# Kernel optimization log

Hardware: AMD Instinct MI355X
Metric: run time of the kernel (lower is better)

The kernel has to match this reference:

```python
import jax, jax.numpy as jnp
import numpy as np
from jax import lax

E = 3  # num_experts

def _maxpool2(x):
    return lax.reduce_window(x, -jnp.inf, lax.max, (1, 1, 2, 2), (1, 1, 2, 2), 'VALID')

def _mixed_conv(x, experts, routing, stride, pad):
    # per-sample expert-mixed convolution via grouped conv trick
    B, Ci, H, W = x.shape
    _, Co, _, k, _ = experts.shape
    kern = jnp.einsum('be,eoikl->boikl', routing, experts).reshape(B * Co, Ci, k, k)
    y = lax.conv_general_dilated(
        x.reshape(1, B * Ci, H, W), kern, (stride, stride),
        [(pad, pad), (pad, pad)],
        dimension_numbers=('NCHW', 'OIHW', 'NCHW'),
        feature_group_count=B)
    return y.reshape(B, Co, y.shape[2], y.shape[3])

def _dyres_conv(x, experts, rw, rb, stride=1, pad=1):
    # DyRes mode 'A': routing from avg-pool + spatial-std descriptors, softmax over experts
    avg = x.mean((2, 3))
    std = x.std((2, 3))
    r = jax.nn.softmax((avg + std) @ rw.T + rb, axis=-1)  # [B, E]
    return _mixed_conv(x, experts, r, stride, pad)

def _cond_conv(x, experts, rw, rb, stride=1, pad=1):
    # CondConv: sigmoid routing from global average pool
    r = jax.nn.sigmoid(x.mean((2, 3)) @ rw.T + rb)  # [B, E]
    return _mixed_conv(x, experts, r, stride, pad)

def _conv_init(key, co, ci, k):
    return jax.random.normal(key, (E, co, ci, k, k), jnp.float32) * np.sqrt(2.0 / (ci * k * k)).astype(np.float32)

def setup_inputs() -> dict:
    key = jax.random.key(0)
    ks = jax.random.split(key, 20)
    B = 512
    d = {}
    d['x'] = jax.random.normal(ks[0], (B, 3, 32, 32), jnp.float32)
    d['dw1'] = _conv_init(ks[1], 64, 3, 3)
    d['rw1'] = jax.random.normal(ks[2], (E, 3), jnp.float32) * 0.1
    d['rb1'] = jnp.zeros((E,), jnp.float32)
    d['dw2'] = _conv_init(ks[3], 192, 64, 3)
    d['rw2'] = jax.random.normal(ks[4], (E, 64), jnp.float32) * 0.1
    d['rb2'] = jnp.zeros((E,), jnp.float32)
    d['dw3'] = _conv_init(ks[5], 384, 192, 3)
    d['rw3'] = jax.random.normal(ks[6], (E, 192), jnp.float32) * 0.1
    d['rb3'] = jnp.zeros((E,), jnp.float32)
    d['cw4'] = _conv_init(ks[7], 256, 384, 3)
    d['cr4w'] = jax.random.normal(ks[8], (E, 384), jnp.float32) * 0.1
    d['cr4b'] = jnp.zeros((E,), jnp.float32)
    d['cw5'] = _conv_init(ks[9], 256, 256, 3)
    d['cr5w'] = jax.random.normal(ks[10], (E, 256), jnp.float32) * 0.1
    d['cr5b'] = jnp.zeros((E,), jnp.float32)
    d['fw1'] = jax.random.normal(ks[11], (4096, 1024), jnp.float32) * np.sqrt(2.0 / 1024).astype(np.float32)
    d['fb1'] = jnp.zeros((4096,), jnp.float32)
    d['fw2'] = jax.random.normal(ks[12], (4096, 4096), jnp.float32) * np.sqrt(2.0 / 4096).astype(np.float32)
    d['fb2'] = jnp.zeros((4096,), jnp.float32)
    d['fw3'] = jax.random.normal(ks[13], (100, 4096), jnp.float32) * np.sqrt(1.0 / 4096).astype(np.float32)
    d['fb3'] = jnp.zeros((100,), jnp.float32)
    return d

def reference(x, dw1, rw1, rb1, dw2, rw2, rb2, dw3, rw3, rb3,
              cw4, cr4w, cr4b, cw5, cr5w, cr5b,
              fw1, fb1, fw2, fb2, fw3, fb3):
    h = jax.nn.relu(_dyres_conv(x, dw1, rw1, rb1, stride=2))   # [B,64,16,16]
    h = _maxpool2(h)                                           # [B,64,8,8]
    h = jax.nn.relu(_dyres_conv(h, dw2, rw2, rb2))             # [B,192,8,8]
    h = _maxpool2(h)                                           # [B,192,4,4]
    h = jax.nn.relu(_dyres_conv(h, dw3, rw3, rb3))             # [B,384,4,4]
    h = jax.nn.relu(_cond_conv(h, cw4, cr4w, cr4b))            # [B,256,4,4]
    h = jax.nn.relu(_cond_conv(h, cw5, cr5w, cr5b))            # [B,256,4,4]
    h = _maxpool2(h)                                           # [B,256,2,2]
    h = h.reshape(h.shape[0], -1)                              # [B,1024]
    h = jax.nn.relu(h @ fw1.T + fb1)
    h = jax.nn.relu(h @ fw2.T + fb2)
    return h @ fw3.T + fb3                                     # [B,100]
```

## Files before the change

kernel.cpp:

```cpp
#include <hip/hip_runtime.h>
#include <math.h>


typedef unsigned short u16;
typedef unsigned int u32;
typedef short bf16x8 __attribute__((ext_vector_type(8)));
typedef short bf16x4 __attribute__((ext_vector_type(4)));
typedef float f32x4 __attribute__((ext_vector_type(4)));

__device__ __forceinline__ u16 bf16_rne(float f) {
    u32 u = __float_as_uint(f);
    return (u16)((u + 0x7fffu + ((u >> 16) & 1u)) >> 16);
}
__device__ __forceinline__ u32 packsplit(float v) {
    u16 h = bf16_rne(v);
    float hf = __uint_as_float((u32)h << 16);
    u16 l = bf16_rne(v - hf);
    return ((u32)h << 16) | l;
}
__device__ __forceinline__ float unpackf(u32 p) {
    return __uint_as_float(p & 0xffff0000u) + __uint_as_float(p << 16);
}
__device__ __forceinline__ int xcd_swz(int bid, int n) {
    if ((n & 7) != 0) return bid;
    int cpx = n >> 3;
    return (bid & 7) * cpx + (bid >> 3);
}

#if __has_builtin(__builtin_amdgcn_mfma_f32_16x16x16bf16_1k)
__device__ __forceinline__ f32x4 mfma16(bf16x4 a, bf16x4 b, f32x4 c) {
    return __builtin_amdgcn_mfma_f32_16x16x16bf16_1k(a, b, c, 0, 0, 0);
}
#else
__device__ __forceinline__ f32x4 mfma16(bf16x4 a, bf16x4 b, f32x4 c) {
    bf16x8 az = {a[0], a[1], a[2], a[3], (short)0, (short)0, (short)0, (short)0};
    bf16x8 bz = {b[0], b[1], b[2], b[3], (short)0, (short)0, (short)0, (short)0};
    return __builtin_amdgcn_mfma_f32_16x16x32_bf16(az, bz, c, 0, 0, 0);
}
#endif

__global__ __launch_bounds__(256)
void wsplit_kernel(const float* __restrict__ W, u16* __restrict__ whi,
                   u16* __restrict__ wlo, int total, int Kper, int Kpad)
{
    int idx = blockIdx.x * 256 + threadIdx.x;
    if (idx >= total) return;
    int r = idx / Kpad, k = idx - r * Kpad;
    float v = (k < Kper) ? W[(size_t)r * Kper + k] : 0.f;
    u16 h = bf16_rne(v);
    whi[idx] = h;
    wlo[idx] = bf16_rne(v - __uint_as_float((u32)h << 16));
}

__global__ __launch_bounds__(256)
void wsplit_cl_kernel(const float* __restrict__ W, u16* __restrict__ whi,
                      u16* __restrict__ wlo, int total, int Ci)
{
    int idx = blockIdx.x * 256 + threadIdx.x;
    if (idx >= total) return;
    int Kper = 9 * Ci;
    int r = idx / Kper, kp = idx - r * Kper;
    int cell = kp / Ci, ci = kp - cell * Ci;
    float v = W[(size_t)r * Kper + ci * 9 + cell];
    u16 h = bf16_rne(v);
    whi[idx] = h;
    wlo[idx] = bf16_rne(v - __uint_as_float((u32)h << 16));
}

__global__ __launch_bounds__(64)
void stats_kernel(const float* __restrict__ actv, float* __restrict__ s,
                  int C, int HW, int use_std)
{
    int idx = blockIdx.x;
    size_t base = (size_t)idx * HW;
    int lane = threadIdx.x;
    float sum = 0.f, sq = 0.f;
    const float* p = actv + base;
    for (int i = lane; i < HW; i += 64) { float v = p[i]; sum += v; sq += v * v; }
#pragma unroll
    for (int off = 32; off > 0; off >>= 1) {
        sum += __shfl_down(sum, off);
        sq  += __shfl_down(sq, off);
    }
    if (lane == 0) {
        float inv = 1.f / (float)HW;
        float mean = sum * inv;
        float var = sq * inv - mean * mean;
        float outv = mean;
        if (use_std) outv += sqrtf(fmaxf(var, 0.f));
        s[idx] = outv;
    }
}

__global__ __launch_bounds__(384)
void stats_cl_kernel(const u32* __restrict__ act, float* __restrict__ s,
                     int H2, int W2, int C, int use_std)
{
    int b = blockIdx.x, c = threadIdx.x;
    int Hin = H2 - 2, Win = W2 - 2;
    float sum = 0.f, sq = 0.f;
    for (int h = 0; h < Hin; ++h)
        for (int w = 0; w < Win; ++w) {
            float v = unpackf(act[(((size_t)b * H2 + h + 1) * W2 + w + 1) * C + c]);
            sum += v; sq += v * v;
        }
    float inv = 1.f / (float)(Hin * Win);
    float mean = sum * inv;
    float var = sq * inv - mean * mean;
    float outv = mean;
    if (use_std) outv += sqrtf(fmaxf(var, 0.f));
    s[b * C + c] = outv;
}

__global__ __launch_bounds__(64)
void routing_kernel(const float* __restrict__ s, const float* __restrict__ rw,
                    const float* __restrict__ rb, float* __restrict__ r,
                    int C, int softmax_mode)
{
    int b = blockIdx.x;
    int lane = threadIdx.x;
    float d0 = 0.f, d1 = 0.f, d2 = 0.f;
    for (int c = lane; c < C; c += 64) {
        float sv = s[b * C + c];
        d0 += sv * rw[c];
        d1 += sv * rw[C + c];
        d2 += sv * rw[2 * C + c];
    }
#pragma unroll
    for (int off = 32; off > 0; off >>= 1) {
        d0 += __shfl_down(d0, off);
        d1 += __shfl_down(d1, off);
        d2 += __shfl_down(d2, off);
    }
    if (lane == 0) {
        d0 += rb[0]; d1 += rb[1]; d2 += rb[2];
        if (softmax_mode) {
            float mx = fmaxf(d0, fmaxf(d1, d2));
            float e0 = expf(d0 - mx), e1 = expf(d1 - mx), e2 = expf(d2 - mx);
            float inv = 1.f / (e0 + e1 + e2);
            r[b * 3 + 0] = e0 * inv;
            r[b * 3 + 1] = e1 * inv;
            r[b * 3 + 2] = e2 * inv;
        } else {
            r[b * 3 + 0] = 1.f / (1.f + expf(-d0));
            r[b * 3 + 1] = 1.f / (1.f + expf(-d1));
            r[b * 3 + 2] = 1.f / (1.f + expf(-d2));
        }
    }
}

template<int CI, int H2, int W2, int LGS, int LGOW>
__global__ __launch_bounds__(256, 3)
void cgemm_cl_kernel(const u16* __restrict__ Whi, const u16* __restrict__ Wlo,
                     const u32* __restrict__ Bpk, const float* __restrict__ rptr,
                     float* __restrict__ Cout, int M, int N, int Kper, int Kchunk)
{
    __shared__ __align__(16) u16 Ah[2][128 * 20], Al[2][128 * 20];
    __shared__ __align__(16) u16 Bh[2][128 * 20], Bl[2][128 * 20];
    const int tid = threadIdx.x;
    const int bx = xcd_swz(blockIdx.x, gridDim.x);
    const int n0 = bx << 7, m0 = blockIdx.y << 7;
    const int kq0 = blockIdx.z * Kchunk;

    const int rowA = tid >> 1, kh8 = (tid & 1) << 3;
    const int nBr = tid >> 1, kOffB = (tid & 1) << 3;

    const int nn = n0 + nBr;
    const int bB = nn >> LGS;
    const int sidx = nn & ((1 << LGS) - 1);
    const int oh = sidx >> LGOW, ow = sidx & ((1 << LGOW) - 1);
    const long nBase = ((long)(bB * H2 + oh) * W2 + ow) * CI;
    const float rsB0 = rptr[bB * 3 + 0];
    const float rsB1 = rptr[bB * 3 + 1];
    const float rsB2 = rptr[bB * 3 + 2];

    const int lane = tid & 63, wv = tid >> 6;
    const int lm = lane & 15, qd = lane >> 4;
    const int wm = (wv & 1) << 6, wn = (wv >> 1) << 6;

    f32x4 acc[4][4];
#pragma unroll
    for (int i = 0; i < 4; ++i)
#pragma unroll
        for (int j = 0; j < 4; ++j)
            acc[i][j] = (f32x4){0.f, 0.f, 0.f, 0.f};

    const int mg = m0 + rowA;
    const int nkz = Kchunk >> 4;
    const int NS = 3 * nkz;

    int eL = 0, kL = kq0;
    uint4 pAh, pAl;
    uint4 pQ0, pQ1;

    auto LOAD = [&]() {
        size_t aOff = ((size_t)(eL * M + mg)) * Kper + kL + kh8;
        pAh = *(const uint4*)(Whi + aOff);
        pAl = *(const uint4*)(Wlo + aOff);
        int k = kL + kOffB;
        int cell = k / CI;
        int ci0 = k - cell * CI;
        int kh = (cell * 11) >> 5;
        int kw = cell - kh * 3;
        const u32* bp = Bpk + (nBase + (long)((kh * W2 + kw) * CI + ci0));
        pQ0 = *(const uint4*)bp;
        pQ1 = *(const uint4*)(bp + 4);
    };
    auto ADV = [&]() {
        kL += 16;
        if (kL == kq0 + Kchunk) { kL = kq0; ++eL; }
    };
    auto STORE = [&](int buf, float rs) {
        *(uint4*)(&Ah[buf][rowA * 20 + kh8]) = pAh;
        *(uint4*)(&Al[buf][rowA * 20 + kh8]) = pAl;
        u32 qv[8] = {pQ0.x, pQ0.y, pQ0.z, pQ0.w, pQ1.x, pQ1.y, pQ1.z, pQ1.w};
        u32 sv[8];
#pragma unroll
        for (int j = 0; j < 8; ++j)
            sv[j] = packsplit(unpackf(qv[j]) * rs);
        u32 hw[4], lw[4];
#pragma unroll
        for (int j = 0; j < 4; ++j) {
            u32 p0 = sv[2 * j], p1 = sv[2 * j + 1];
            hw[j] = (p0 >> 16) | (p1 & 0xffff0000u);
            lw[j] = (p0 & 0xffffu) | (p1 << 16);
        }
        *(uint4*)(&Bh[buf][nBr * 20 + kOffB]) = make_uint4(hw[0], hw[1], hw[2], hw[3]);
        *(uint4*)(&Bl[buf][nBr * 20 + kOffB]) = make_uint4(lw[0], lw[1], lw[2], lw[3]);
    };
    auto COMPUTE = [&](int buf) {
        bf16x4 ah[4], al[4];
#pragma unroll
        for (int mi = 0; mi < 4; ++mi) {
            int off = (wm + mi * 16 + lm) * 20 + qd * 4;
            ah[mi] = *(const bf16x4*)(&Ah[buf][off]);
            al[mi] = *(const bf16x4*)(&Al[buf][off]);
        }
        __builtin_amdgcn_s_setprio(1);
#pragma unroll
        for (int ni = 0; ni < 4; ++ni) {
            int off = (wn + ni * 16 + lm) * 20 + qd * 4;
            bf16x4 bh = *(const bf16x4*)(&Bh[buf][off]);
            bf16x4 bl = *(const bf16x4*)(&Bl[buf][off]);
#pragma unroll
            for (int mi = 0; mi < 4; ++mi) {
                f32x4 c = acc[mi][ni];
                c = mfma16(al[mi], bh, c);
                c = mfma16(ah[mi], bl, c);
                c = mfma16(ah[mi], bh, c);
                acc[mi][ni] = c;
            }
        }
        __builtin_amdgcn_s_setprio(0);
    };

    LOAD(); ADV();
    int s = 0, buf = 0;
#pragma unroll
    for (int e = 0; e < 3; ++e) {
        const float rs = (e == 0) ? rsB0 : ((e == 1) ? rsB1 : rsB2);
        for (int t = 0; t < nkz; ++t) {
            STORE(buf, rs);
            if (s + 1 < NS) { LOAD(); ADV(); }
            asm volatile("s_waitcnt lgkmcnt(0)\n\ts_barrier" ::: "memory");
            COMPUTE(buf);
            buf ^= 1; ++s;
        }
    }

    const bool atom = (gridDim.z > 1);
#pragma unroll
    for (int ni = 0; ni < 4; ++ni) {
        int n = n0 + wn + ni * 16 + lm;
#pragma unroll
        for (int mi = 0; mi < 4; ++mi)
#pragma unroll
            for (int r = 0; r < 4; ++r) {
                int m = m0 + wm + mi * 16 + qd * 4 + r;
                if (m >= M) continue;
                float v = acc[mi][ni][r];
                if (atom) atomicAdd(&Cout[(size_t)n * M + m], v);
                else      Cout[(size_t)n * M + m] = v;
            }
    }
}

__global__ __launch_bounds__(256, 2)
void cgemm_l1_kernel(const u16* __restrict__ Whi, const u16* __restrict__ Wlo,
                     const u32* __restrict__ Bpk, const float* __restrict__ rptr,
                     float* __restrict__ Cout, int M, int N)
{
    __shared__ __align__(16) u16 Ah[2][128 * 40], Al[2][128 * 40];
    __shared__ __align__(16) u16 Bh[2][128 * 40], Bl[2][128 * 40];
    const int tid = threadIdx.x;
    const int bx = xcd_swz(blockIdx.x, gridDim.x);
    const int n0 = bx << 7;
    const int Kper = 27, Kpad = 32;
    const int H = 32, W = 32;

    const int rowA = tid >> 1, kh16 = (tid & 1) << 4;
    const int nB = tid & 127, kOff = (tid >> 7) << 4;

    const int nn = n0 + nB;
    const int bB = nn >> 8;
    const int sidx = nn & 255;
    const int ohs = (sidx >> 4) * 2 - 1;
    const int ows = (sidx & 15) * 2 - 1;
    const long nBase = (long)bB * 3072 + (long)ohs * W + ows;

    const int lane = tid & 63, wv = tid >> 6;
    const int lm = lane & 15, qd = lane >> 4;
    const int wm = (wv & 1) << 6, wn = (wv >> 1) << 6;

    float rsv[3][4];
#pragma unroll
    for (int ni = 0; ni < 4; ++ni) {
        int n = n0 + wn + ni * 16 + lm;
        int b = n >> 8;
#pragma unroll
        for (int e = 0; e < 3; ++e) rsv[e][ni] = rptr[b * 3 + e];
    }

    f32x4 acc[4][4], accS[4][4];
#pragma unroll
    for (int i = 0; i < 4; ++i)
#pragma unroll
        for (int j = 0; j < 4; ++j) {
            acc[i][j]  = (f32x4){0.f, 0.f, 0.f, 0.f};
            accS[i][j] = (f32x4){0.f, 0.f, 0.f, 0.f};
        }

    const int mg = rowA;
    int eL = 0;
    uint4 pA0, pA1, pA2, pA3;
    u32 pB[16];

    auto LOAD = [&]() {
        size_t aOff = ((size_t)(eL * M + mg)) * Kpad + kh16;
        const u16* hp = Whi + aOff;
        const u16* lp = Wlo + aOff;
        pA0 = *(const uint4*)hp; pA1 = *(const uint4*)(hp + 8);
        pA2 = *(const uint4*)lp; pA3 = *(const uint4*)(lp + 8);
#pragma unroll
        for (int j = 0; j < 16; ++j) {
            int k = kOff + j;
            int ci = (int)((unsigned)k / 9u);
            int r9 = k - ci * 9;
            int kh = (int)(((unsigned)r9 * 11u) >> 5);
            int kw = r9 - kh * 3;
            int ih = ohs + kh, iw = ows + kw;
            u32 p = 0;
            if (k < Kper && (unsigned)ih < (unsigned)H && (unsigned)iw < (unsigned)W)
                p = Bpk[nBase + (long)ci * 1024 + kh * W + kw];
            pB[j] = p;
        }
    };
    auto STORE = [&](int buf) {
        *(uint4*)(&Ah[buf][rowA * 40 + kh16])     = pA0;
        *(uint4*)(&Ah[buf][rowA * 40 + kh16 + 8]) = pA1;
        *(uint4*)(&Al[buf][rowA * 40 + kh16])     = pA2;
        *(uint4*)(&Al[buf][rowA * 40 + kh16 + 8]) = pA3;
        u32 hw[8], lw[8];
#pragma unroll
        for (int j = 0; j < 8; ++j) {
            u32 p0 = pB[2 * j], p1 = pB[2 * j + 1];
            hw[j] = (p0 >> 16) | (p1 & 0xffff0000u);
            lw[j] = (p0 & 0xffffu) | (p1 << 16);
        }
        *(uint4*)(&Bh[buf][nB * 40 + kOff])     = make_uint4(hw[0], hw[1], hw[2], hw[3]);
        *(uint4*)(&Bh[buf][nB * 40 + kOff + 8]) = make_uint4(hw[4], hw[5], hw[6], hw[7]);
        *(uint4*)(&Bl[buf][nB * 40 + kOff])     = make_uint4(lw[0], lw[1], lw[2], lw[3]);
        *(uint4*)(&Bl[buf][nB * 40 + kOff + 8]) = make_uint4(lw[4], lw[5], lw[6], lw[7]);
    };
    auto COMPUTE = [&](int buf) {
        bf16x8 ah[4], al[4];
#pragma unroll
        for (int mi = 0; mi < 4; ++mi) {
            int row = wm + mi * 16 + lm;
            ah[mi] = *(const bf16x8*)(&Ah[buf][row * 40 + qd * 8]);
            al[mi] = *(const bf16x8*)(&Al[buf][row * 40 + qd * 8]);
        }
        __builtin_amdgcn_s_setprio(1);
#pragma unroll
        for (int ni = 0; ni < 4; ++ni) {
            int row = wn + ni * 16 + lm;
            bf16x8 bh = *(const bf16x8*)(&Bh[buf][row * 40 + qd * 8]);
            bf16x8 bl = *(const bf16x8*)(&Bl[buf][row * 40 + qd * 8]);
#pragma unroll
            for (int mi = 0; mi < 4; ++mi) {
                f32x4 c = acc[mi][ni];
                c = __builtin_amdgcn_mfma_f32_16x16x32_bf16(al[mi], bh, c, 0, 0, 0);
                c = __builtin_amdgcn_mfma_f32_16x16x32_bf16(ah[mi], bl, c, 0, 0, 0);
                c = __builtin_amdgcn_mfma_f32_16x16x32_bf16(ah[mi], bh, c, 0, 0, 0);
                acc[mi][ni] = c;
            }
        }
        __builtin_amdgcn_s_setprio(0);
    };

    LOAD(); ++eL;
    int buf = 0;
#pragma unroll
    for (int e = 0; e < 3; ++e) {
        STORE(buf);
        if (e < 2) { LOAD(); ++eL; }
        asm volatile("s_waitcnt lgkmcnt(0)\n\ts_barrier" ::: "memory");
        COMPUTE(buf);
        buf ^= 1;
#pragma unroll
        for (int mi = 0; mi < 4; ++mi)
#pragma unroll
            for (int ni = 0; ni < 4; ++ni) {
                accS[mi][ni] += acc[mi][ni] * rsv[e][ni];
                acc[mi][ni] = (f32x4){0.f, 0.f, 0.f, 0.f};
            }
    }

#pragma unroll
    for (int ni = 0; ni < 4; ++ni) {
        int n = n0 + wn + ni * 16 + lm;
#pragma unroll
        for (int mi = 0; mi < 4; ++mi)
#pragma unroll
            for (int r = 0; r < 4; ++r) {
                int m = wm + mi * 16 + qd * 4 + r;
                if (m >= M) continue;
                Cout[(size_t)n * M + m] = accS[mi][ni][r];
            }
    }
}

template<int BIAS, int TROUT>
__global__ __launch_bounds__(256, 2)
void mgemm_kernel(const u16* __restrict__ Whi, const u16* __restrict__ Wlo,
                  const u32* __restrict__ Bpk, const float* __restrict__ bias,
                  float* __restrict__ Cout,
                  int M, int N, int Kpad, int Kchunk)
{
    __shared__ __align__(16) u16 Ah[2][128 * 40], Al[2][128 * 40];
    __shared__ __align__(16) u32 Bp[2][128 * 36];
    const int tid = threadIdx.x;
    const int n0 = blockIdx.x << 7, m0 = blockIdx.y << 7;
    const int bz = blockIdx.z;
    const int kq0 = bz * Kchunk;
    const int kEnd = kq0 + Kchunk;

    const int rowA = tid >> 1, kh16 = (tid & 1) << 4;
    const int nB = tid & 127, kOff = (tid >> 7) << 4;

    const int lane = tid & 63, wv = tid >> 6;
    const int lm = lane & 15, qd = lane >> 4;
    const int wm = (wv & 1) << 6, wn = (wv >> 1) << 6;

    f32x4 acc[4][4];
#pragma unroll
    for (int i = 0; i < 4; ++i)
#pragma unroll
        for (int j = 0; j < 4; ++j)
            acc[i][j] = (f32x4){0.f, 0.f, 0.f, 0.f};

    const int mg = m0 + rowA;
    uint4 pA0, pA1, pA2, pA3;
    uint4 pQ0, pQ1, pQ2, pQ3;

    auto LOAD = [&](int kq) {
        if (mg < M) {
            const u16* hp = Whi + (size_t)mg * Kpad + kq + kh16;
            const u16* lp = Wlo + (size_t)mg * Kpad + kq + kh16;
            pA0 = *(const uint4*)hp; pA1 = *(const uint4*)(hp + 8);
            pA2 = *(const uint4*)lp; pA3 = *(const uint4*)(lp + 8);
        } else {
            pA0 = make_uint4(0,0,0,0); pA1 = make_uint4(0,0,0,0);
            pA2 = make_uint4(0,0,0,0); pA3 = make_uint4(0,0,0,0);
        }
        const u32* bp = Bpk + (size_t)(n0 + nB) * Kpad + kq + kOff;
        pQ0 = *(const uint4*)bp;
        pQ1 = *(const uint4*)(bp + 4);
        pQ2 = *(const uint4*)(bp + 8);
        pQ3 = *(const uint4*)(bp + 12);
    };
    auto STORE = [&](int buf) {
        *(uint4*)(&Ah[buf][rowA * 40 + kh16])     = pA0;
        *(uint4*)(&Ah[buf][rowA * 40 + kh16 + 8]) = pA1;
        *(uint4*)(&Al[buf][rowA * 40 + kh16])     = pA2;
        *(uint4*)(&Al[buf][rowA * 40 + kh16 + 8]) = pA3;
        u32* bp = &Bp[buf][nB * 36 + kOff];
        *(uint4*)(bp)      = pQ0;
        *(uint4*)(bp + 4)  = pQ1;
        *(uint4*)(bp + 8)  = pQ2;
        *(uint4*)(bp + 12) = pQ3;
    };
    auto COMPUTE = [&](int buf) {
        bf16x8 ah[4], al[4];
#pragma unroll
        for (int mi = 0; mi < 4; ++mi) {
            int row = wm + mi * 16 + lm;
            ah[mi] = *(const bf16x8*)(&Ah[buf][row * 40 + qd * 8]);
            al[mi] = *(const bf16x8*)(&Al[buf][row * 40 + qd * 8]);
        }
        __builtin_amdgcn_s_setprio(1);
#pragma unroll
        for (int ni = 0; ni < 4; ++ni) {
            const u32* bp = &Bp[buf][(wn + ni * 16 + lm) * 36 + qd * 8];
            uint4 p0 = *(const uint4*)bp;
            uint4 p1 = *(const uint4*)(bp + 4);
            union { u32 w[4]; bf16x8 v; } bh, bl;
            bh.w[0] = (p0.x >> 16) | (p0.y & 0xffff0000u);
            bl.w[0] = (p0.x & 0xffffu) | (p0.y << 16);
            bh.w[1] = (p0.z >> 16) | (p0.w & 0xffff0000u);
            bl.w[1] = (p0.z & 0xffffu) | (p0.w << 16);
            bh.w[2] = (p1.x >> 16) | (p1.y & 0xffff0000u);
            bl.w[2] = (p1.x & 0xffffu) | (p1.y << 16);
            bh.w[3] = (p1.z >> 16) | (p1.w & 0xffff0000u);
            bl.w[3] = (p1.z & 0xffffu) | (p1.w << 16);
#pragma unroll
            for (int mi = 0; mi < 4; ++mi) {
                f32x4 c = acc[mi][ni];
                c = __builtin_amdgcn_mfma_f32_16x16x32_bf16(al[mi], bh.v, c, 0, 0, 0);
                c = __builtin_amdgcn_mfma_f32_16x16x32_bf16(ah[mi], bl.v, c, 0, 0, 0);
                c = __builtin_amdgcn_mfma_f32_16x16x32_bf16(ah[mi], bh.v, c, 0, 0, 0);
                acc[mi][ni] = c;
            }
        }
        __builtin_amdgcn_s_setprio(0);
    };

    LOAD(kq0);
    int buf = 0;
    for (int kq = kq0; kq < kEnd; kq += 32) {
        STORE(buf);
        if (kq + 32 < kEnd) LOAD(kq + 32);
        asm volatile("s_waitcnt lgkmcnt(0)\n\ts_barrier" ::: "memory");
        COMPUTE(buf);
        buf ^= 1;
    }

#pragma unroll
    for (int ni = 0; ni < 4; ++ni) {
        int n = n0 + wn + ni * 16 + lm;
        if (n >= N) continue;
#pragma unroll
        for (int mi = 0; mi < 4; ++mi)
#pragma unroll
            for (int r = 0; r < 4; ++r) {
                int m = m0 + wm + mi * 16 + qd * 4 + r;
                if (m >= M) continue;
                float v = acc[mi][ni][r];
                if (BIAS && bz == 0) v += bias[m];
                if (TROUT) atomicAdd(&Cout[(size_t)n * M + m], v);
                else       atomicAdd(&Cout[(size_t)m * N + n], v);
            }
    }
}

__global__ __launch_bounds__(256)
void pack_kernel(const float* __restrict__ in, u32* __restrict__ outp, int count)
{
    int i = blockIdx.x * 256 + threadIdx.x;
    if (i >= count) return;
    outp[i] = packsplit(in[i]);
}

__global__ __launch_bounds__(256)
void pool_pack_cl_kernel(const float* __restrict__ in, u32* __restrict__ outp,
                         int Bn, int Hin, int Win, int C)
{
    int OH = Hin >> 1, OW = Win >> 1, H2 = OH + 2, W2 = OW + 2;
    int total = Bn * H2 * W2 * C;
    int i = blockIdx.x * 256 + threadIdx.x;
    if (i >= total) return;
    int c = i % C; int t = i / C;
    int w = t % W2; t /= W2;
    int h = t % H2; int b = t / H2;
    u32 pv = 0;
    if (h >= 1 && h <= OH && w >= 1 && w <= OW) {
        int oh = h - 1, ow = w - 1;
        const float* p = in + (((size_t)b * Hin + 2 * oh) * Win + 2 * ow) * C + c;
        size_t rs = (size_t)Win * C;
        float v = fmaxf(fmaxf(p[0], p[C]), fmaxf(p[rs], p[rs + C]));
        pv = packsplit(fmaxf(v, 0.f));
    }
    outp[i] = pv;
}

__global__ __launch_bounds__(256)
void pack_cl_kernel(const float* __restrict__ in, u32* __restrict__ outp,
                    int Bn, int Hin, int Win, int C)
{
    int H2 = Hin + 2, W2 = Win + 2;
    int total = Bn * H2 * W2 * C;
    int i = blockIdx.x * 256 + threadIdx.x;
    if (i >= total) return;
    int c = i % C; int t = i / C;
    int w = t % W2; t /= W2;
    int h = t % H2; int b = t / H2;
    u32 pv = 0;
    if (h >= 1 && h <= Hin && w >= 1 && w <= Win) {
        float v = in[(((size_t)b * Hin + (h - 1)) * Win + (w - 1)) * C + c];
        pv = packsplit(fmaxf(v, 0.f));
    }
    outp[i] = pv;
}

__global__ __launch_bounds__(256)
void pool_flatten_cl_kernel(const float* __restrict__ in, u32* __restrict__ outp)
{
    int i = blockIdx.x * 256 + threadIdx.x;
    if (i >= 512 * 1024) return;
    int b = i >> 10;
    int f = i & 1023;
    int c = f >> 2, sp = f & 3;
    int oh = sp >> 1, ow = sp & 1;
    const float* p = in + (((size_t)b * 4 + 2 * oh) * 4 + 2 * ow) * 256 + c;
    float v = fmaxf(fmaxf(p[0], p[256]), fmaxf(p[1024], p[1024 + 256]));
    outp[i] = packsplit(fmaxf(v, 0.f));
}

__global__ __launch_bounds__(256)
void tp_pack_kernel(const float* __restrict__ in, u32* __restrict__ outp,
                    int Mt, int Nt)
{
    __shared__ float t[32][33];
    int tx = threadIdx.x & 31, ty = threadIdx.x >> 5;
    int mB = blockIdx.x << 5, nB = blockIdx.y << 5;
#pragma unroll
    for (int i = 0; i < 4; ++i) {
        int mm = ty + i * 8;
        t[mm][tx] = in[(size_t)(mB + mm) * Nt + nB + tx];
    }
    __syncthreads();
#pragma unroll
    for (int i = 0; i < 4; ++i) {
        int nn = ty + i * 8;
        float v = fmaxf(t[tx][nn], 0.f);
        outp[(size_t)(nB + nn) * Mt + mB + tx] = packsplit(v);
    }
}

extern "C" void kernel_launch(void* const* d_in, const int* in_sizes, int n_in,
                              void* d_out, int out_size, void* d_ws, size_t ws_size,
                              hipStream_t stream)
{
    const float* x    = (const float*)d_in[0];
    const float* dw1  = (const float*)d_in[1];
    const float* rw1  = (const float*)d_in[2];
    const float* rb1  = (const float*)d_in[3];
    const float* dw2  = (const float*)d_in[4];
    const float* rw2  = (const float*)d_in[5];
    const float* rb2  = (const float*)d_in[6];
    const float* dw3  = (const float*)d_in[7];
    const float* rw3  = (const float*)d_in[8];
    const float* rb3  = (const float*)d_in[9];
    const float* cw4  = (const float*)d_in[10];
    const float* cr4w = (const float*)d_in[11];
    const float* cr4b = (const float*)d_in[12];
    const float* cw5  = (const float*)d_in[13];
    const float* cr5w = (const float*)d_in[14];
    const float* cr5b = (const float*)d_in[15];
    const float* fw1  = (const float*)d_in[16];
    const float* fb1  = (const float*)d_in[17];
    const float* fw2  = (const float*)d_in[18];
    const float* fb2  = (const float*)d_in[19];
    const float* fw3  = (const float*)d_in[20];
    const float* fb3  = (const float*)d_in[21];
    float* out = (float*)d_out;

    float* ws    = (float*)d_ws;
    float* r1    = ws;
    float* r2    = r1 + 1536;
    float* r3    = r2 + 1536;
    float* r4    = r3 + 1536;
    float* r5    = r4 + 1536;
    float* sdesc = ws + 8192 + 65536;
    const size_t REGION = 18874368;
    float* region = sdesc + 196608;
    float* slab   = region;
    u32*   a3u    = (u32*)(region + 4194304);
    u16*   regEnd = (u16*)(region + REGION);
    u32*   P1     = (u32*)(region + REGION);

    u16 *w1h = regEnd - 2*(size_t)6144,     *w1l = regEnd - (size_t)6144;
    u16 *w2h = regEnd - 2*(size_t)331776,   *w2l = regEnd - (size_t)331776;
    u16 *w3h = regEnd - 2*(size_t)1990656,  *w3l = regEnd - (size_t)1990656;
    u16 *w4h = regEnd - 2*(size_t)2654208,  *w4l = regEnd - (size_t)2654208;
    u16 *w5h = regEnd - 2*(size_t)1769472,  *w5l = regEnd - (size_t)1769472;
    u16 *f1h = regEnd - 2*(size_t)4194304,  *f1l = regEnd - (size_t)4194304;
    u16 *f2h = regEnd - 2*(size_t)16777216, *f2l = regEnd - (size_t)16777216;
    u16 *f3h = regEnd - 2*(size_t)409600,   *f3l = regEnd - (size_t)409600;

    u32* xpk   = P1;
    u32* a1    = P1;
    u32* a2    = P1;
    u32* a4    = P1;
    u32* hTpk  = P1;
    u32* f1pkT = P1 + 1048576;
    u32* f2pkT = P1 + 3145728;

    const int B = 512;

    pack_kernel<<<6144, 256, 0, stream>>>(x, xpk, 1572864);

    wsplit_kernel<<<24, 256, 0, stream>>>(dw1, w1h, w1l, 6144, 27, 32);
    stats_kernel<<<B * 3, 64, 0, stream>>>(x, sdesc, 3, 1024, 1);
    routing_kernel<<<B, 64, 0, stream>>>(sdesc, rw1, rb1, r1, 3, 1);
    cgemm_l1_kernel<<<dim3(1024, 1, 1), 256, 0, stream>>>(
        w1h, w1l, xpk, r1, slab, 64, 131072);
    pool_pack_cl_kernel<<<12800, 256, 0, stream>>>(slab, a1, B, 16, 16, 64);

    wsplit_cl_kernel<<<1296, 256, 0, stream>>>(dw2, w2h, w2l, 331776, 64);
    stats_cl_kernel<<<B, 64, 0, stream>>>(a1, sdesc, 10, 10, 64, 1);
    routing_kernel<<<B, 64, 0, stream>>>(sdesc, rw2, rb2, r2, 64, 1);
    hipMemsetAsync(slab, 0, (size_t)192 * 32768 * 4, stream);
    cgemm_cl_kernel<64, 10, 10, 6, 3><<<dim3(256, 2, 2), 256, 0, stream>>>(
        w2h, w2l, a1, r2, slab, 192, 32768, 576, 288);
    pool_pack_cl_kernel<<<13824, 256, 0, stream>>>(slab, a2, B, 8, 8, 192);

    wsplit_cl_kernel<<<7776, 256, 0, stream>>>(dw3, w3h, w3l, 1990656, 192);
    stats_cl_kernel<<<B, 192, 0, stream>>>(a2, sdesc, 6, 6, 192, 1);
    routing_kernel<<<B, 64, 0, stream>>>(sdesc, rw3, rb3, r3, 192, 1);
    hipMemsetAsync(slab, 0, (size_t)8192 * 384 * 4, stream);
    cgemm_cl_kernel<192, 6, 6, 4, 2><<<dim3(64, 3, 4), 256, 0, stream>>>(
        w3h, w3l, a2, r3, slab, 384, 8192, 1728, 432);
    pack_cl_kernel<<<27648, 256, 0, stream>>>(slab, a3u, B, 4, 4, 384);

    wsplit_cl_kernel<<<10368, 256, 0, stream>>>(cw4, w4h, w4l, 2654208, 384);
    stats_cl_kernel<<<B, 384, 0, stream>>>(a3u, sdesc, 6, 6, 384, 0);
    routing_kernel<<<B, 64, 0, stream>>>(sdesc, cr4w, cr4b, r4, 384, 0);
    hipMemsetAsync(slab, 0, (size_t)8192 * 256 * 4, stream);
    cgemm_cl_kernel<384, 6, 6, 4, 2><<<dim3(64, 2, 6), 256, 0, stream>>>(
        w4h, w4l, a3u, r4, slab, 256, 8192, 3456, 576);
    pack_cl_kernel<<<18432, 256, 0, stream>>>(slab, a4, B, 4, 4, 256);

    wsplit_cl_kernel<<<6912, 256, 0, stream>>>(cw5, w5h, w5l, 1769472, 256);
    stats_cl_kernel<<<B, 256, 0, stream>>>(a4, sdesc, 6, 6, 256, 0);
    routing_kernel<<<B, 64, 0, stream>>>(sdesc, cr5w, cr5b, r5, 256, 0);
    hipMemsetAsync(slab, 0, (size_t)8192 * 256 * 4, stream);
    cgemm_cl_kernel<256, 6, 6, 4, 2><<<dim3(64, 2, 6), 256, 0, stream>>>(
        w5h, w5l, a4, r5, slab, 256, 8192, 2304, 384);

    pool_flatten_cl_kernel<<<2048, 256, 0, stream>>>(slab, hTpk);

    wsplit_kernel<<<16384, 256, 0, stream>>>(fw1, f1h, f1l, 4194304, 1024, 1024);
    hipMemsetAsync(slab, 0, (size_t)4096 * 512 * 4, stream);
    mgemm_kernel<1, 0><<<dim3(4, 32, 8), 256, 0, stream>>>(
        f1h, f1l, hTpk, fb1, slab, 4096, 512, 1024, 128);
    tp_pack_kernel<<<dim3(128, 16), 256, 0, stream>>>(slab, f1pkT, 4096, 512);

    wsplit_kernel<<<65536, 256, 0, stream>>>(fw2, f2h, f2l, 16777216, 4096, 4096);
    hipMemsetAsync(slab, 0, (size_t)4096 * 512 * 4, stream);
    mgemm_kernel<1, 0><<<dim3(4, 32, 8), 256, 0, stream>>>(
        f2h, f2l, f1pkT, fb2, slab, 4096, 512, 4096, 512);
    tp_pack_kernel<<<dim3(128, 16), 256, 0, stream>>>(slab, f2pkT, 4096, 512);

    wsplit_kernel<<<1600, 256, 0, stream>>>(fw3, f3h, f3l, 409600, 4096, 4096);
    hipMemsetAsync(out, 0, (size_t)512 * 100 * 4, stream);
    mgemm_kernel<1, 1><<<dim3(4, 1, 32), 256, 0, stream>>>(
        f3h, f3l, f2pkT, fb3, out, 100, 512, 4096, 128);
}
```

Before: 1.807 ms.

## Use K=32 bf16 MFMA with packed hi/lo weights in conv GEMMs

The conv-layer GEMMs now store weights as packed hi/lo u32 words, produced by a new split kernel. Shared-memory tiles hold packed u32 values that are split into bf16x8 operands at fragment load, so each step can use 16x16x32 MFMAs instead of 16x16x16. The M tile shrinks to 64, the K step doubles to 32, and split-K counts and grids are retuned. Layer 2 drops split-K, along with its memset and atomics. The change cuts MFMA instruction count and global load count, but adds unpacking ALU work in the inner loop and lowers per-block reuse of B.

```diff
diff --git a/kernel.cpp b/kernel.cpp
--- a/kernel.cpp
+++ b/kernel.cpp
@@ -5,7 +5,6 @@
 typedef unsigned short u16;
 typedef unsigned int u32;
 typedef short bf16x8 __attribute__((ext_vector_type(8)));
-typedef short bf16x4 __attribute__((ext_vector_type(4)));
 typedef float f32x4 __attribute__((ext_vector_type(4)));
 
 __device__ __forceinline__ u16 bf16_rne(float f) {
@@ -26,18 +25,6 @@
     int cpx = n >> 3;
     return (bid & 7) * cpx + (bid >> 3);
 }
-
-#if __has_builtin(__builtin_amdgcn_mfma_f32_16x16x16bf16_1k)
-__device__ __forceinline__ f32x4 mfma16(bf16x4 a, bf16x4 b, f32x4 c) {
-    return __builtin_amdgcn_mfma_f32_16x16x16bf16_1k(a, b, c, 0, 0, 0);
-}
-#else
-__device__ __forceinline__ f32x4 mfma16(bf16x4 a, bf16x4 b, f32x4 c) {
-    bf16x8 az = {a[0], a[1], a[2], a[3], (short)0, (short)0, (short)0, (short)0};
-    bf16x8 bz = {b[0], b[1], b[2], b[3], (short)0, (short)0, (short)0, (short)0};
-    return __builtin_amdgcn_mfma_f32_16x16x32_bf16(az, bz, c, 0, 0, 0);
-}
-#endif
 
 __global__ __launch_bounds__(256)
 void wsplit_kernel(const float* __restrict__ W, u16* __restrict__ whi,
@@ -53,18 +40,19 @@
 }
 
 __global__ __launch_bounds__(256)
-void wsplit_cl_kernel(const float* __restrict__ W, u16* __restrict__ whi,
-                      u16* __restrict__ wlo, int total, int Ci)
+void wsplit_clp_kernel(const float* __restrict__ W, u32* __restrict__ wp,
+                       int total, int Ci, int Kpad)
 {
     int idx = blockIdx.x * 256 + threadIdx.x;
     if (idx >= total) return;
     int Kper = 9 * Ci;
-    int r = idx / Kper, kp = idx - r * Kper;
-    int cell = kp / Ci, ci = kp - cell * Ci;
-    float v = W[(size_t)r * Kper + ci * 9 + cell];
-    u16 h = bf16_rne(v);
-    whi[idx] = h;
-    wlo[idx] = bf16_rne(v - __uint_as_float((u32)h << 16));
+    int r = idx / Kpad, k = idx - r * Kpad;
+    u32 p = 0;
+    if (k < Kper) {
+        int cell = k / Ci, ci = k - cell * Ci;
+        p = packsplit(W[(size_t)r * Kper + ci * 9 + cell]);
+    }
+    wp[idx] = p;
 }
 
 __global__ __launch_bounds__(64)
@@ -151,19 +139,19 @@
 
 template<int CI, int H2, int W2, int LGS, int LGOW>
 __global__ __launch_bounds__(256, 3)
-void cgemm_cl_kernel(const u16* __restrict__ Whi, const u16* __restrict__ Wlo,
-                     const u32* __restrict__ Bpk, const float* __restrict__ rptr,
-                     float* __restrict__ Cout, int M, int N, int Kper, int Kchunk)
-{
-    __shared__ __align__(16) u16 Ah[2][128 * 20], Al[2][128 * 20];
-    __shared__ __align__(16) u16 Bh[2][128 * 20], Bl[2][128 * 20];
+void cgemm_cl_kernel(const u32* __restrict__ Apk, const u32* __restrict__ Bpk,
+                     const float* __restrict__ rptr, float* __restrict__ Cout,
+                     int M, int N, int Kper, int Kchunk)
+{
+    __shared__ __align__(16) u32 ApS[2][64 * 34];
+    __shared__ __align__(16) u32 BpS[2][128 * 34];
     const int tid = threadIdx.x;
     const int bx = xcd_swz(blockIdx.x, gridDim.x);
-    const int n0 = bx << 7, m0 = blockIdx.y << 7;
+    const int n0 = bx << 7, m0 = blockIdx.y << 6;
     const int kq0 = blockIdx.z * Kchunk;
 
-    const int rowA = tid >> 1, kh8 = (tid & 1) << 3;
-    const int nBr = tid >> 1, kOffB = (tid & 1) << 3;
+    const int rowA = tid >> 2, kA = (tid & 3) << 3;
+    const int nBr = tid >> 1, kB = (tid & 1) << 4;
 
     const int nn = n0 + nBr;
     const int bB = nn >> LGS;
@@ -176,28 +164,27 @@
 
     const int lane = tid & 63, wv = tid >> 6;
     const int lm = lane & 15, qd = lane >> 4;
-    const int wm = (wv & 1) << 6, wn = (wv >> 1) << 6;
-
-    f32x4 acc[4][4];
-#pragma unroll
-    for (int i = 0; i < 4; ++i)
+    const int wm = (wv & 1) << 5, wn = (wv >> 1) << 6;
+
+    f32x4 acc[2][4];
+#pragma unroll
+    for (int i = 0; i < 2; ++i)
 #pragma unroll
         for (int j = 0; j < 4; ++j)
             acc[i][j] = (f32x4){0.f, 0.f, 0.f, 0.f};
 
-    const int mg = m0 + rowA;
-    const int nkz = Kchunk >> 4;
+    const int nkz = Kchunk >> 5;
     const int NS = 3 * nkz;
 
     int eL = 0, kL = kq0;
-    uint4 pAh, pAl;
-    uint4 pQ0, pQ1;
+    uint4 pA0, pA1;
+    uint4 pQ0, pQ1, pQ2, pQ3;
 
     auto LOAD = [&]() {
-        size_t aOff = ((size_t)(eL * M + mg)) * Kper + kL + kh8;
-        pAh = *(const uint4*)(Whi + aOff);
-        pAl = *(const uint4*)(Wlo + aOff);
-        int k = kL + kOffB;
+        const u32* ap = Apk + ((size_t)(eL * M + m0 + rowA)) * Kper + kL + kA;
+        pA0 = *(const uint4*)ap;
+        pA1 = *(const uint4*)(ap + 4);
+        int k = kL + kB;
         int cell = k / CI;
         int ci0 = k - cell * CI;
         int kh = (cell * 11) >> 5;
@@ -205,49 +192,68 @@
         const u32* bp = Bpk + (nBase + (long)((kh * W2 + kw) * CI + ci0));
         pQ0 = *(const uint4*)bp;
         pQ1 = *(const uint4*)(bp + 4);
+        pQ2 = *(const uint4*)(bp + 8);
+        pQ3 = *(const uint4*)(bp + 12);
     };
     auto ADV = [&]() {
-        kL += 16;
+        kL += 32;
         if (kL == kq0 + Kchunk) { kL = kq0; ++eL; }
     };
     auto STORE = [&](int buf, float rs) {
-        *(uint4*)(&Ah[buf][rowA * 20 + kh8]) = pAh;
-        *(uint4*)(&Al[buf][rowA * 20 + kh8]) = pAl;
-        u32 qv[8] = {pQ0.x, pQ0.y, pQ0.z, pQ0.w, pQ1.x, pQ1.y, pQ1.z, pQ1.w};
-        u32 sv[8];
-#pragma unroll
-        for (int j = 0; j < 8; ++j)
+        u32* ap = &ApS[buf][rowA * 34 + kA];
+        *(uint4*)(ap)     = pA0;
+        *(uint4*)(ap + 4) = pA1;
+        u32 qv[16] = {pQ0.x, pQ0.y, pQ0.z, pQ0.w, pQ1.x, pQ1.y, pQ1.z, pQ1.w,
+                      pQ2.x, pQ2.y, pQ2.z, pQ2.w, pQ3.x, pQ3.y, pQ3.z, pQ3.w};
+        u32 sv[16];
+#pragma unroll
+        for (int j = 0; j < 16; ++j)
             sv[j] = packsplit(unpackf(qv[j]) * rs);
-        u32 hw[4], lw[4];
-#pragma unroll
-        for (int j = 0; j < 4; ++j) {
-            u32 p0 = sv[2 * j], p1 = sv[2 * j + 1];
-            hw[j] = (p0 >> 16) | (p1 & 0xffff0000u);
-            lw[j] = (p0 & 0xffffu) | (p1 << 16);
-        }
-        *(uint4*)(&Bh[buf][nBr * 20 + kOffB]) = make_uint4(hw[0], hw[1], hw[2], hw[3]);
-        *(uint4*)(&Bl[buf][nBr * 20 + kOffB]) = make_uint4(lw[0], lw[1], lw[2], lw[3]);
+        u32* bp = &BpS[buf][nBr * 34 + kB];
+        *(uint4*)(bp)      = make_uint4(sv[0], sv[1], sv[2], sv[3]);
+        *(uint4*)(bp + 4)  = make_uint4(sv[4], sv[5], sv[6], sv[7]);
+        *(uint4*)(bp + 8)  = make_uint4(sv[8], sv[9], sv[10], sv[11]);
+        *(uint4*)(bp + 12) = make_uint4(sv[12], sv[13], sv[14], sv[15]);
     };
     auto COMPUTE = [&](int buf) {
-        bf16x4 ah[4], al[4];
-#pragma unroll
-        for (int mi = 0; mi < 4; ++mi) {
-            int off = (wm + mi * 16 + lm) * 20 + qd * 4;
-            ah[mi] = *(const bf16x4*)(&Ah[buf][off]);
-            al[mi] = *(const bf16x4*)(&Al[buf][off]);
+        bf16x8 ah[2], al[2];
+#pragma unroll
+        for (int mi = 0; mi < 2; ++mi) {
+            const u32* ap = &ApS[buf][(wm + mi * 16 + lm) * 34 + qd * 8];
+            uint4 q0 = *(const uint4*)ap;
+            uint4 q1 = *(const uint4*)(ap + 4);
+            union { u32 w[4]; bf16x8 v; } h, l;
+            h.w[0] = (q0.x >> 16) | (q0.y & 0xffff0000u);
+            l.w[0] = (q0.x & 0xffffu) | (q0.y << 16);
+            h.w[1] = (q0.z >> 16) | (q0.w & 0xffff0000u);
+            l.w[1] = (q0.z & 0xffffu) | (q0.w << 16);
+            h.w[2] = (q1.x >> 16) | (q1.y & 0xffff0000u);
+            l.w[2] = (q1.x & 0xffffu) | (q1.y << 16);
+            h.w[3] = (q1.z >> 16) | (q1.w & 0xffff0000u);
+            l.w[3] = (q1.z & 0xffffu) | (q1.w << 16);
+            ah[mi] = h.v; al[mi] = l.v;
         }
         __builtin_amdgcn_s_setprio(1);
 #pragma unroll
         for (int ni = 0; ni < 4; ++ni) {
-            int off = (wn + ni * 16 + lm) * 20 + qd * 4;
-            bf16x4 bh = *(const bf16x4*)(&Bh[buf][off]);
-            bf16x4 bl = *(const bf16x4*)(&Bl[buf][off]);
-#pragma unroll
-            for (int mi = 0; mi < 4; ++mi) {
+            const u32* bp = &BpS[buf][(wn + ni * 16 + lm) * 34 + qd * 8];
+            uint4 p0 = *(const uint4*)bp;
+            uint4 p1 = *(const uint4*)(bp + 4);
+            union { u32 w[4]; bf16x8 v; } bh, bl;
+            bh.w[0] = (p0.x >> 16) | (p0.y & 0xffff0000u);
+            bl.w[0] = (p0.x & 0xffffu) | (p0.y << 16);
+            bh.w[1] = (p0.z >> 16) | (p0.w & 0xffff0000u);
+            bl.w[1] = (p0.z & 0xffffu) | (p0.w << 16);
+            bh.w[2] = (p1.x >> 16) | (p1.y & 0xffff0000u);
+            bl.w[2] = (p1.x & 0xffffu) | (p1.y << 16);
+            bh.w[3] = (p1.z >> 16) | (p1.w & 0xffff0000u);
+            bl.w[3] = (p1.z & 0xffffu) | (p1.w << 16);
+#pragma unroll
+            for (int mi = 0; mi < 2; ++mi) {
                 f32x4 c = acc[mi][ni];
-                c = mfma16(al[mi], bh, c);
-                c = mfma16(ah[mi], bl, c);
-                c = mfma16(ah[mi], bh, c);
+                c = __builtin_amdgcn_mfma_f32_16x16x32_bf16(al[mi], bh.v, c, 0, 0, 0);
+                c = __builtin_amdgcn_mfma_f32_16x16x32_bf16(ah[mi], bl.v, c, 0, 0, 0);
+                c = __builtin_amdgcn_mfma_f32_16x16x32_bf16(ah[mi], bh.v, c, 0, 0, 0);
                 acc[mi][ni] = c;
             }
         }
@@ -273,11 +279,10 @@
     for (int ni = 0; ni < 4; ++ni) {
         int n = n0 + wn + ni * 16 + lm;
 #pragma unroll
-        for (int mi = 0; mi < 4; ++mi)
+        for (int mi = 0; mi < 2; ++mi)
 #pragma unroll
             for (int r = 0; r < 4; ++r) {
                 int m = m0 + wm + mi * 16 + qd * 4 + r;
-                if (m >= M) continue;
                 float v = acc[mi][ni][r];
                 if (atom) atomicAdd(&Cout[(size_t)n * M + m], v);
                 else      Cout[(size_t)n * M + m] = v;
@@ -680,10 +685,10 @@
     u32*   P1     = (u32*)(region + REGION);
 
     u16 *w1h = regEnd - 2*(size_t)6144,     *w1l = regEnd - (size_t)6144;
-    u16 *w2h = regEnd - 2*(size_t)331776,   *w2l = regEnd - (size_t)331776;
-    u16 *w3h = regEnd - 2*(size_t)1990656,  *w3l = regEnd - (size_t)1990656;
-    u16 *w4h = regEnd - 2*(size_t)2654208,  *w4l = regEnd - (size_t)2654208;
-    u16 *w5h = regEnd - 2*(size_t)1769472,  *w5l = regEnd - (size_t)1769472;
+    u32 *w2p = (u32*)(regEnd - 2*(size_t)331776);
+    u32 *w3p = (u32*)(regEnd - 2*(size_t)1990656);
+    u32 *w4p = (u32*)(regEnd - 2*(size_t)2654208);
+    u32 *w5p = (u32*)(regEnd - 2*(size_t)1769472);
     u16 *f1h = regEnd - 2*(size_t)4194304,  *f1l = regEnd - (size_t)4194304;
     u16 *f2h = regEnd - 2*(size_t)16777216, *f2l = regEnd - (size_t)16777216;
     u16 *f3h = regEnd - 2*(size_t)409600,   *f3l = regEnd - (size_t)409600;
@@ -707,36 +712,35 @@
         w1h, w1l, xpk, r1, slab, 64, 131072);
     pool_pack_cl_kernel<<<12800, 256, 0, stream>>>(slab, a1, B, 16, 16, 64);
 
-    wsplit_cl_kernel<<<1296, 256, 0, stream>>>(dw2, w2h, w2l, 331776, 64);
+    wsplit_clp_kernel<<<1296, 256, 0, stream>>>(dw2, w2p, 331776, 64, 576);
     stats_cl_kernel<<<B, 64, 0, stream>>>(a1, sdesc, 10, 10, 64, 1);
     routing_kernel<<<B, 64, 0, stream>>>(sdesc, rw2, rb2, r2, 64, 1);
-    hipMemsetAsync(slab, 0, (size_t)192 * 32768 * 4, stream);
-    cgemm_cl_kernel<64, 10, 10, 6, 3><<<dim3(256, 2, 2), 256, 0, stream>>>(
-        w2h, w2l, a1, r2, slab, 192, 32768, 576, 288);
+    cgemm_cl_kernel<64, 10, 10, 6, 3><<<dim3(256, 3, 1), 256, 0, stream>>>(
+        w2p, a1, r2, slab, 192, 32768, 576, 576);
     pool_pack_cl_kernel<<<13824, 256, 0, stream>>>(slab, a2, B, 8, 8, 192);
 
-    wsplit_cl_kernel<<<7776, 256, 0, stream>>>(dw3, w3h, w3l, 1990656, 192);
+    wsplit_clp_kernel<<<7776, 256, 0, stream>>>(dw3, w3p, 1990656, 192, 1728);
     stats_cl_kernel<<<B, 192, 0, stream>>>(a2, sdesc, 6, 6, 192, 1);
     routing_kernel<<<B, 64, 0, stream>>>(sdesc, rw3, rb3, r3, 192, 1);
     hipMemsetAsync(slab, 0, (size_t)8192 * 384 * 4, stream);
-    cgemm_cl_kernel<192, 6, 6, 4, 2><<<dim3(64, 3, 4), 256, 0, stream>>>(
-        w3h, w3l, a2, r3, slab, 384, 8192, 1728, 432);
+    cgemm_cl_kernel<192, 6, 6, 4, 2><<<dim3(64, 6, 2), 256, 0, stream>>>(
+        w3p, a2, r3, slab, 384, 8192, 1728, 864);
     pack_cl_kernel<<<27648, 256, 0, stream>>>(slab, a3u, B, 4, 4, 384);
 
-    wsplit_cl_kernel<<<10368, 256, 0, stream>>>(cw4, w4h, w4l, 2654208, 384);
+    wsplit_clp_kernel<<<10368, 256, 0, stream>>>(cw4, w4p, 2654208, 384, 3456);
     stats_cl_kernel<<<B, 384, 0, stream>>>(a3u, sdesc, 6, 6, 384, 0);
     routing_kernel<<<B, 64, 0, stream>>>(sdesc, cr4w, cr4b, r4, 384, 0);
     hipMemsetAsync(slab, 0, (size_t)8192 * 256 * 4, stream);
-    cgemm_cl_kernel<384, 6, 6, 4, 2><<<dim3(64, 2, 6), 256, 0, stream>>>(
-        w4h, w4l, a3u, r4, slab, 256, 8192, 3456, 576);
+    cgemm_cl_kernel<384, 6, 6, 4, 2><<<dim3(64, 4, 3), 256, 0, stream>>>(
+        w4p, a3u, r4, slab, 256, 8192, 3456, 1152);
     pack_cl_kernel<<<18432, 256, 0, stream>>>(slab, a4, B, 4, 4, 256);
 
-    wsplit_cl_kernel<<<6912, 256, 0, stream>>>(cw5, w5h, w5l, 1769472, 256);
+    wsplit_clp_kernel<<<6912, 256, 0, stream>>>(cw5, w5p, 1769472, 256, 2304);
     stats_cl_kernel<<<B, 256, 0, stream>>>(a4, sdesc, 6, 6, 256, 0);
     routing_kernel<<<B, 64, 0, stream>>>(sdesc, cr5w, cr5b, r5, 256, 0);
     hipMemsetAsync(slab, 0, (size_t)8192 * 256 * 4, stream);
-    cgemm_cl_kernel<256, 6, 6, 4, 2><<<dim3(64, 2, 6), 256, 0, stream>>>(
-        w5h, w5l, a4, r5, slab, 256, 8192, 2304, 384);
+    cgemm_cl_kernel<256, 6, 6, 4, 2><<<dim3(64, 4, 3), 256, 0, stream>>>(
+        w5p, a4, r5, slab, 256, 8192, 2304, 768);
 
     pool_flatten_cl_kernel<<<2048, 256, 0, stream>>>(slab, hTpk);
 
```

Result: slower. 2.698 ms (+49.3%).
